# Kernel tuning notes

Hardware: AMD Instinct MI355X
Metric: run time of the kernel (lower is better)

## Reference

```python
import jax, jax.numpy as jnp
import numpy as np
from jax import lax

EPS = 1e-4


def setup_inputs() -> dict:
    key = jax.random.key(0)
    k1, k2, k3 = jax.random.split(key, 3)
    B, L, M, D = 4, 4096, 1024, 2048
    chunked_states = jax.random.normal(k1, (B, M, D), dtype=jnp.float32)
    boundary_prob = jax.random.uniform(k2, (B, L, 2), dtype=jnp.float32)
    boundary_mask = jax.random.randint(k3, (B, L), 0, 2).astype(jnp.bool_)
    return {
        "chunked_states": chunked_states,
        "boundary_prob": boundary_prob,
        "boundary_mask": boundary_mask,
    }


def _ema_scan(x, p):
    """out[0]=x[0]; out[t]=p[t]*x[t]+(1-p[t])*out[t-1] via associative scan.
    x: (B,M,D), p: (B,M)."""
    a = (1.0 - p).at[:, 0].set(0.0)                 # (B, M)
    b = (p[..., None] * x).at[:, 0].set(x[:, 0])    # (B, M, D)

    def combine(c1, c2):
        a1, b1 = c1
        a2, b2 = c2
        return a1 * a2, a2[..., None] * b1 + b2

    _, out = lax.associative_scan(combine, (a, b), axis=1)
    return out


def reference(chunked_states, boundary_prob, boundary_mask):
    B, L = boundary_mask.shape
    M, D = chunked_states.shape[1], chunked_states.shape[2]

    p = jnp.clip(boundary_prob[..., -1].astype(jnp.float32), EPS, 1.0 - EPS)  # (B, L)

    # Stable-in-effect sort: boundary tokens keep index, non-boundary shifted by +L
    token_idx = jnp.arange(L, dtype=jnp.int32)[None, :] + (~boundary_mask).astype(jnp.int32) * L
    sorted_indices = jnp.argsort(token_idx, axis=1)[:, :M]                    # (B, M)
    p_chunked = jnp.take_along_axis(p, sorted_indices, axis=1)                # (B, M)

    expanded_chunked = _ema_scan(chunked_states, p_chunked)                   # (B, M, D)

    chunk_indices = jnp.clip(jnp.cumsum(boundary_mask.astype(jnp.int32), axis=1) - 1, 0, M - 1)  # (B, L)
    expanded_states = jnp.take_along_axis(expanded_chunked, chunk_indices[..., None], axis=1)    # (B, L, D)
    return expanded_states
```

## Files before the change

### kernel.cpp

```cpp
#include <hip/hip_runtime.h>

#define BB 4
#define LL 4096
#define MM 1024
#define DD 2048
#define SEG 128
#define SM 8
#define NSCAN (BB * SEG * 2)
#define BCAST 1024
#define EXIT_EPS 1e-7f

typedef float f32x4 __attribute__((ext_vector_type(4)));

__global__ __launch_bounds__(1024) void prep_kernel(
    const float* __restrict__ bprob,
    const int*   __restrict__ bmask,
    float* __restrict__ p_chunked,
    int*   __restrict__ row_start,
    float* __restrict__ Ppref)
{
    const int b   = blockIdx.x;
    const int tid = threadIdx.x;
    const int lane = tid & 63;
    const int wid  = tid >> 6;

    __shared__ int wsum[16];
    __shared__ int s_total;
    __shared__ int rs_sh[MM + 1];

    rs_sh[tid] = LL;
    if (tid == 0) rs_sh[MM] = LL;

    int4 mv = reinterpret_cast<const int4*>(bmask + b * LL)[tid];
    int ms[4] = { mv.x, mv.y, mv.z, mv.w };
    int s = ms[0] + ms[1] + ms[2] + ms[3];

    int v = s;
    #pragma unroll
    for (int off = 1; off < 64; off <<= 1) {
        int u = __shfl_up(v, off, 64);
        if (lane >= off) v += u;
    }
    if (lane == 63) wsum[wid] = v;
    __syncthreads();
    if (tid == 0) {
        int acc = 0;
        #pragma unroll
        for (int w = 0; w < 16; ++w) { int t = wsum[w]; wsum[w] = acc; acc += t; }
        s_total = acc;
    }
    __syncthreads();

    const int NB = s_total;
    int e = (v - s) + wsum[wid];

    const int base_l = tid * 4;
    #pragma unroll
    for (int j = 0; j < 4; ++j) {
        int l = base_l + j;
        int m = ms[j];
        int incl = e + m;
        int ci = incl - 1;
        ci = ci < 0 ? 0 : (ci > MM - 1 ? MM - 1 : ci);
        int pci = e - 1;
        pci = pci < 0 ? 0 : (pci > MM - 1 ? MM - 1 : pci);
        if (l == 0 || ci != pci) rs_sh[ci] = l;
        int pos = m ? e : (NB + (l - e));
        if (pos < MM) {
            float2 pv = *reinterpret_cast<const float2*>(
                bprob + ((size_t)b * LL + l) * 2);
            float p = fminf(fmaxf(pv.y, 1e-4f), 1.0f - 1e-4f);
            p_chunked[b * MM + pos] = p;
        }
        e = incl;
    }
    __syncthreads();

    row_start[b * (MM + 1) + tid] = rs_sh[tid];
    if (tid == 0) row_start[b * (MM + 1) + MM] = rs_sh[MM];

    {
        int t = tid;
        float p = p_chunked[b * MM + t];
        float a = (t == 0) ? 0.0f : (1.0f - p);
        float pr = a;
        #pragma unroll
        for (int off = 1; off < SM; off <<= 1) {
            float u = __shfl_up(pr, off, SM);
            if ((t & (SM - 1)) >= off) pr *= u;
        }
        Ppref[b * MM + t] = pr;
    }
}

__global__ __launch_bounds__(256) void seglast_kernel(
    const float* __restrict__ x,
    const float* __restrict__ p_chunked,
    float* __restrict__ seglast)
{
    const int tid = threadIdx.x;
    const int dsl = blockIdx.x;
    const int d0  = dsl * 1024 + tid * 4;
    const int seg = blockIdx.y;
    const int b   = blockIdx.z;
    const int t0  = seg * SM;

    __shared__ float sp[SM];
    if (tid < SM) sp[tid] = p_chunked[b * MM + t0 + tid];
    __syncthreads();

    const size_t base = ((size_t)b * MM + t0) * DD + d0;

    f32x4 prev = {0.0f, 0.0f, 0.0f, 0.0f};
    #pragma unroll
    for (int i = 0; i < SM; ++i) {
        float p = sp[i];
        float ac, bc;
        if (i == 0) { ac = (seg == 0) ? 0.0f : (1.0f - p); bc = (seg == 0) ? 1.0f : p; }
        else        { ac = 1.0f - p; bc = p; }
        f32x4 xt = *reinterpret_cast<const f32x4*>(x + base + (size_t)i * DD);
        prev = ac * prev + bc * xt;
    }
    *reinterpret_cast<f32x4*>(
        seglast + (((size_t)(b * 2 + dsl) * SEG + seg)) * 1024 + tid * 4) = prev;
}

static __device__ __forceinline__ f32x4 lookback(
    const float* __restrict__ seglast, const float* __restrict__ sPf,
    int bd, int seg, int tid)
{
    f32x4 c = {0.0f, 0.0f, 0.0f, 0.0f};
    float mult = 1.0f;
    const float* base = seglast + (size_t)bd * SEG * 1024 + tid * 4;
    for (int j = seg - 1; j >= 0; --j) {
        f32x4 sl = *reinterpret_cast<const f32x4*>(base + (size_t)j * 1024);
        c += mult * sl;
        mult *= sPf[j];
        if (mult < EXIT_EPS) break;
    }
    return c;
}

__global__ __launch_bounds__(256) void scatter_kernel(
    const float* __restrict__ x,
    const float* __restrict__ p_chunked,
    const float* __restrict__ Ppref,
    const int*   __restrict__ row_start,
    const float* __restrict__ seglast,
    float* __restrict__ out)
{
    const int id  = blockIdx.x;
    const int tid = threadIdx.x;

    __shared__ float sPf[SEG];

    if (id < NSCAN) {
        const int dsl = id & 1;
        const int seg = (id >> 1) & (SEG - 1);
        const int b   = id >> 8;
        const int d0  = dsl * 1024 + tid * 4;
        const int t0  = seg * SM;
        const int bd  = b * 2 + dsl;

        __shared__ float sp[SM];
        __shared__ int   rs[SM + 1];
        if (tid < SM) sp[tid] = p_chunked[b * MM + t0 + tid];
        if (tid < SM + 1) rs[tid] = row_start[b * (MM + 1) + t0 + tid];
        if (tid < SEG) sPf[tid] = Ppref[b * MM + tid * SM + SM - 1];
        __syncthreads();

        f32x4 prev = lookback(seglast, sPf, bd, seg, tid);

        const size_t base = ((size_t)b * MM + t0) * DD + d0;
        #pragma unroll
        for (int i = 0; i < SM; ++i) {
            float p = sp[i];
            float ac, bc;
            if (i == 0) { ac = (seg == 0) ? 0.0f : (1.0f - p); bc = (seg == 0) ? 1.0f : p; }
            else        { ac = 1.0f - p; bc = p; }
            f32x4 xt = *reinterpret_cast<const f32x4*>(x + base + (size_t)i * DD);
            prev = ac * prev + bc * xt;

            int t = t0 + i;
            if (t == MM - 1) continue;
            int l0r = rs[i], l1r = rs[i + 1];
            for (int l = l0r; l < l1r; ++l)
                *reinterpret_cast<f32x4*>(out + ((size_t)b * LL + l) * DD + d0) = prev;
        }
    } else {
        const int j    = id - NSCAN;
        const int g    = j & 7;
        const int chnk = j >> 3;
        const int b    = g >> 1;
        const int dsl  = g & 1;
        const int d0   = dsl * 1024 + tid * 4;
        const int bd   = b * 2 + dsl;

        if (tid < SEG) sPf[tid] = Ppref[b * MM + tid * SM + SM - 1];
        __syncthreads();

        f32x4 v = lookback(seglast, sPf, bd, SEG, tid);

        const int l0 = row_start[b * (MM + 1) + (MM - 1)];
        for (int l = l0 + chnk; l < LL; l += 128)
            *reinterpret_cast<f32x4*>(out + ((size_t)b * LL + l) * DD + d0) = v;
    }
}

extern "C" void kernel_launch(void* const* d_in, const int* in_sizes, int n_in,
                              void* d_out, int out_size, void* d_ws, size_t ws_size,
                              hipStream_t stream) {
    const float* x     = (const float*)d_in[0];
    const float* bprob = (const float*)d_in[1];
    const int*   bmask = (const int*)d_in[2];

    float* out = (float*)d_out;

    float* seglast   = (float*)d_ws;
    float* p_chunked = seglast + (size_t)BB * 2 * SEG * 1024;
    float* Ppref     = p_chunked + BB * MM;
    int*   row_start = (int*)(Ppref + BB * MM);

    prep_kernel<<<BB, 1024, 0, stream>>>(bprob, bmask, p_chunked, row_start, Ppref);
    seglast_kernel<<<dim3(2, SEG, BB), 256, 0, stream>>>(x, p_chunked, seglast);
    scatter_kernel<<<NSCAN + BCAST, 256, 0, stream>>>(
        x, p_chunked, Ppref, row_start, seglast, out);
}
```

Baseline: 44.21 us.

## Drop seglast kernel; recompute segment carries by rescanning x in lookback

```diff
diff --git a/kernel.cpp b/kernel.cpp
--- a/kernel.cpp
+++ b/kernel.cpp
@@ -93,47 +93,32 @@
     }
 }
 
-__global__ __launch_bounds__(256) void seglast_kernel(
-    const float* __restrict__ x,
-    const float* __restrict__ p_chunked,
-    float* __restrict__ seglast)
-{
-    const int tid = threadIdx.x;
-    const int dsl = blockIdx.x;
-    const int d0  = dsl * 1024 + tid * 4;
-    const int seg = blockIdx.y;
-    const int b   = blockIdx.z;
-    const int t0  = seg * SM;
-
-    __shared__ float sp[SM];
-    if (tid < SM) sp[tid] = p_chunked[b * MM + t0 + tid];
-    __syncthreads();
-
-    const size_t base = ((size_t)b * MM + t0) * DD + d0;
-
+static __device__ __forceinline__ f32x4 seg_scan(
+    const float* __restrict__ x, const float* __restrict__ sp8,
+    int b, int j, int d0)
+{
     f32x4 prev = {0.0f, 0.0f, 0.0f, 0.0f};
+    const size_t base = ((size_t)b * MM + j * SM) * DD + d0;
     #pragma unroll
     for (int i = 0; i < SM; ++i) {
-        float p = sp[i];
+        float p = sp8[i];
         float ac, bc;
-        if (i == 0) { ac = (seg == 0) ? 0.0f : (1.0f - p); bc = (seg == 0) ? 1.0f : p; }
+        if (i == 0) { ac = (j == 0) ? 0.0f : (1.0f - p); bc = (j == 0) ? 1.0f : p; }
         else        { ac = 1.0f - p; bc = p; }
         f32x4 xt = *reinterpret_cast<const f32x4*>(x + base + (size_t)i * DD);
         prev = ac * prev + bc * xt;
     }
-    *reinterpret_cast<f32x4*>(
-        seglast + (((size_t)(b * 2 + dsl) * SEG + seg)) * 1024 + tid * 4) = prev;
-}
-
-static __device__ __forceinline__ f32x4 lookback(
-    const float* __restrict__ seglast, const float* __restrict__ sPf,
-    int bd, int seg, int tid)
+    return prev;
+}
+
+static __device__ __forceinline__ f32x4 lookback_rescan(
+    const float* __restrict__ x, const float* __restrict__ spc,
+    const float* __restrict__ sPf, int b, int seg, int d0)
 {
     f32x4 c = {0.0f, 0.0f, 0.0f, 0.0f};
     float mult = 1.0f;
-    const float* base = seglast + (size_t)bd * SEG * 1024 + tid * 4;
     for (int j = seg - 1; j >= 0; --j) {
-        f32x4 sl = *reinterpret_cast<const f32x4*>(base + (size_t)j * 1024);
+        f32x4 sl = seg_scan(x, spc + j * SM, b, j, d0);
         c += mult * sl;
         mult *= sPf[j];
         if (mult < EXIT_EPS) break;
@@ -146,13 +131,13 @@
     const float* __restrict__ p_chunked,
     const float* __restrict__ Ppref,
     const int*   __restrict__ row_start,
-    const float* __restrict__ seglast,
     float* __restrict__ out)
 {
     const int id  = blockIdx.x;
     const int tid = threadIdx.x;
 
     __shared__ float sPf[SEG];
+    __shared__ float spc[MM];
 
     if (id < NSCAN) {
         const int dsl = id & 1;
@@ -160,21 +145,20 @@
         const int b   = id >> 8;
         const int d0  = dsl * 1024 + tid * 4;
         const int t0  = seg * SM;
-        const int bd  = b * 2 + dsl;
-
-        __shared__ float sp[SM];
-        __shared__ int   rs[SM + 1];
-        if (tid < SM) sp[tid] = p_chunked[b * MM + t0 + tid];
+
+        __shared__ int rs[SM + 1];
+        #pragma unroll
+        for (int k = tid; k < MM; k += 256) spc[k] = p_chunked[b * MM + k];
         if (tid < SM + 1) rs[tid] = row_start[b * (MM + 1) + t0 + tid];
         if (tid < SEG) sPf[tid] = Ppref[b * MM + tid * SM + SM - 1];
         __syncthreads();
 
-        f32x4 prev = lookback(seglast, sPf, bd, seg, tid);
+        f32x4 prev = lookback_rescan(x, spc, sPf, b, seg, d0);
 
         const size_t base = ((size_t)b * MM + t0) * DD + d0;
         #pragma unroll
         for (int i = 0; i < SM; ++i) {
-            float p = sp[i];
+            float p = spc[t0 + i];
             float ac, bc;
             if (i == 0) { ac = (seg == 0) ? 0.0f : (1.0f - p); bc = (seg == 0) ? 1.0f : p; }
             else        { ac = 1.0f - p; bc = p; }
@@ -194,12 +178,13 @@
         const int b    = g >> 1;
         const int dsl  = g & 1;
         const int d0   = dsl * 1024 + tid * 4;
-        const int bd   = b * 2 + dsl;
-
+
+        #pragma unroll
+        for (int k = tid; k < MM; k += 256) spc[k] = p_chunked[b * MM + k];
         if (tid < SEG) sPf[tid] = Ppref[b * MM + tid * SM + SM - 1];
         __syncthreads();
 
-        f32x4 v = lookback(seglast, sPf, bd, SEG, tid);
+        f32x4 v = lookback_rescan(x, spc, sPf, b, SEG, d0);
 
         const int l0 = row_start[b * (MM + 1) + (MM - 1)];
         for (int l = l0 + chnk; l < LL; l += 128)
@@ -216,13 +201,11 @@
 
     float* out = (float*)d_out;
 
-    float* seglast   = (float*)d_ws;
-    float* p_chunked = seglast + (size_t)BB * 2 * SEG * 1024;
+    float* p_chunked = (float*)d_ws;
     float* Ppref     = p_chunked + BB * MM;
     int*   row_start = (int*)(Ppref + BB * MM);
 
     prep_kernel<<<BB, 1024, 0, stream>>>(bprob, bmask, p_chunked, row_start, Ppref);
-    seglast_kernel<<<dim3(2, SEG, BB), 256, 0, stream>>>(x, p_chunked, seglast);
     scatter_kernel<<<NSCAN + BCAST, 256, 0, stream>>>(
-        x, p_chunked, Ppref, row_start, seglast, out);
-}
+        x, p_chunked, Ppref, row_start, out);
+}
```

Result: slower. 47.37 us (+7.2%).

## Merge tail-broadcast blocks into scan blocks and store only per-segment decay products

Applied to the files above, without the earlier changes.

```diff
diff --git a/kernel.cpp b/kernel.cpp
--- a/kernel.cpp
+++ b/kernel.cpp
@@ -7,7 +7,6 @@
 #define SEG 128
 #define SM 8
 #define NSCAN (BB * SEG * 2)
-#define BCAST 1024
 #define EXIT_EPS 1e-7f
 
 typedef float f32x4 __attribute__((ext_vector_type(4)));
@@ -17,7 +16,7 @@
     const int*   __restrict__ bmask,
     float* __restrict__ p_chunked,
     int*   __restrict__ row_start,
-    float* __restrict__ Ppref)
+    float* __restrict__ Pseg)
 {
     const int b   = blockIdx.x;
     const int tid = threadIdx.x;
@@ -89,7 +88,7 @@
             float u = __shfl_up(pr, off, SM);
             if ((t & (SM - 1)) >= off) pr *= u;
         }
-        Ppref[b * MM + t] = pr;
+        if ((t & (SM - 1)) == SM - 1) Pseg[b * SEG + (t >> 3)] = pr;
     }
 }
 
@@ -126,8 +125,8 @@
 }
 
 static __device__ __forceinline__ f32x4 lookback(
-    const float* __restrict__ seglast, const float* __restrict__ sPf,
-    int bd, int seg, int tid)
+    const float* __restrict__ seglast, const float* __restrict__ Pseg,
+    int bd, int b, int seg, int tid)
 {
     f32x4 c = {0.0f, 0.0f, 0.0f, 0.0f};
     float mult = 1.0f;
@@ -135,7 +134,7 @@
     for (int j = seg - 1; j >= 0; --j) {
         f32x4 sl = *reinterpret_cast<const f32x4*>(base + (size_t)j * 1024);
         c += mult * sl;
-        mult *= sPf[j];
+        mult *= Pseg[b * SEG + j];
         if (mult < EXIT_EPS) break;
     }
     return c;
@@ -144,7 +143,7 @@
 __global__ __launch_bounds__(256) void scatter_kernel(
     const float* __restrict__ x,
     const float* __restrict__ p_chunked,
-    const float* __restrict__ Ppref,
+    const float* __restrict__ Pseg,
     const int*   __restrict__ row_start,
     const float* __restrict__ seglast,
     float* __restrict__ out)
@@ -152,57 +151,42 @@
     const int id  = blockIdx.x;
     const int tid = threadIdx.x;
 
-    __shared__ float sPf[SEG];
-
-    if (id < NSCAN) {
-        const int dsl = id & 1;
-        const int seg = (id >> 1) & (SEG - 1);
-        const int b   = id >> 8;
-        const int d0  = dsl * 1024 + tid * 4;
-        const int t0  = seg * SM;
-        const int bd  = b * 2 + dsl;
-
-        __shared__ float sp[SM];
-        __shared__ int   rs[SM + 1];
-        if (tid < SM) sp[tid] = p_chunked[b * MM + t0 + tid];
-        if (tid < SM + 1) rs[tid] = row_start[b * (MM + 1) + t0 + tid];
-        if (tid < SEG) sPf[tid] = Ppref[b * MM + tid * SM + SM - 1];
-        __syncthreads();
-
-        f32x4 prev = lookback(seglast, sPf, bd, seg, tid);
-
-        const size_t base = ((size_t)b * MM + t0) * DD + d0;
-        #pragma unroll
-        for (int i = 0; i < SM; ++i) {
-            float p = sp[i];
-            float ac, bc;
-            if (i == 0) { ac = (seg == 0) ? 0.0f : (1.0f - p); bc = (seg == 0) ? 1.0f : p; }
-            else        { ac = 1.0f - p; bc = p; }
-            f32x4 xt = *reinterpret_cast<const f32x4*>(x + base + (size_t)i * DD);
-            prev = ac * prev + bc * xt;
-
-            int t = t0 + i;
-            if (t == MM - 1) continue;
-            int l0r = rs[i], l1r = rs[i + 1];
-            for (int l = l0r; l < l1r; ++l)
-                *reinterpret_cast<f32x4*>(out + ((size_t)b * LL + l) * DD + d0) = prev;
-        }
-    } else {
-        const int j    = id - NSCAN;
-        const int g    = j & 7;
-        const int chnk = j >> 3;
-        const int b    = g >> 1;
-        const int dsl  = g & 1;
-        const int d0   = dsl * 1024 + tid * 4;
-        const int bd   = b * 2 + dsl;
-
-        if (tid < SEG) sPf[tid] = Ppref[b * MM + tid * SM + SM - 1];
-        __syncthreads();
-
-        f32x4 v = lookback(seglast, sPf, bd, SEG, tid);
-
+    const int dsl = id & 1;
+    const int seg = (id >> 1) & (SEG - 1);
+    const int b   = id >> 8;
+    const int d0  = dsl * 1024 + tid * 4;
+    const int t0  = seg * SM;
+    const int bd  = b * 2 + dsl;
+
+    __shared__ float sp[SM];
+    __shared__ int   rs[SM + 1];
+    if (tid < SM) sp[tid] = p_chunked[b * MM + t0 + tid];
+    if (tid < SM + 1) rs[tid] = row_start[b * (MM + 1) + t0 + tid];
+    __syncthreads();
+
+    f32x4 prev = lookback(seglast, Pseg, bd, b, seg, tid);
+
+    const size_t base = ((size_t)b * MM + t0) * DD + d0;
+    #pragma unroll
+    for (int i = 0; i < SM; ++i) {
+        float p = sp[i];
+        float ac, bc;
+        if (i == 0) { ac = (seg == 0) ? 0.0f : (1.0f - p); bc = (seg == 0) ? 1.0f : p; }
+        else        { ac = 1.0f - p; bc = p; }
+        f32x4 xt = *reinterpret_cast<const f32x4*>(x + base + (size_t)i * DD);
+        prev = ac * prev + bc * xt;
+
+        int t = t0 + i;
+        if (t == MM - 1) continue;
+        int l0r = rs[i], l1r = rs[i + 1];
+        for (int l = l0r; l < l1r; ++l)
+            *reinterpret_cast<f32x4*>(out + ((size_t)b * LL + l) * DD + d0) = prev;
+    }
+
+    {
+        f32x4 v = lookback(seglast, Pseg, bd, b, SEG, tid);
         const int l0 = row_start[b * (MM + 1) + (MM - 1)];
-        for (int l = l0 + chnk; l < LL; l += 128)
+        for (int l = l0 + seg; l < LL; l += SEG)
             *reinterpret_cast<f32x4*>(out + ((size_t)b * LL + l) * DD + d0) = v;
     }
 }
@@ -218,11 +202,11 @@
 
     float* seglast   = (float*)d_ws;
     float* p_chunked = seglast + (size_t)BB * 2 * SEG * 1024;
-    float* Ppref     = p_chunked + BB * MM;
-    int*   row_start = (int*)(Ppref + BB * MM);
-
-    prep_kernel<<<BB, 1024, 0, stream>>>(bprob, bmask, p_chunked, row_start, Ppref);
+    float* Pseg      = p_chunked + BB * MM;
+    int*   row_start = (int*)(Pseg + BB * SEG);
+
+    prep_kernel<<<BB, 1024, 0, stream>>>(bprob, bmask, p_chunked, row_start, Pseg);
     seglast_kernel<<<dim3(2, SEG, BB), 256, 0, stream>>>(x, p_chunked, seglast);
-    scatter_kernel<<<NSCAN + BCAST, 256, 0, stream>>>(
-        x, p_chunked, Ppref, row_start, seglast, out);
-}
+    scatter_kernel<<<NSCAN, 256, 0, stream>>>(
+        x, p_chunked, Pseg, row_start, seglast, out);
+}
```

After: 43.41 us, median of 2. No clear change (-1.8%).
